# Kernel tuning notes

Measured on AMD Instinct MI355X. Metric: run time of the kernel, lower is better.

## Reference

```python
import jax, jax.numpy as jnp
import numpy as np

EPS = 1e-7  # K.epsilon()
ROUTINGS = 3

def squash(v, axis=-1):
    s2 = jnp.sum(jnp.square(v), axis=axis, keepdims=True)
    scale = s2 / (1.0 + s2) / jnp.sqrt(s2 + EPS)
    return scale * v

def setup_inputs() -> dict:
    key = jax.random.key(0)
    k1, k2 = jax.random.split(key)
    B, N, I = 128, 512, 256   # batch, input_num_capsule, input_dim_capsule
    M, D = 32, 16             # num_capsule, dim_capsule
    x = jax.random.normal(k1, (B, N, I), dtype=jnp.float32)
    W = jax.random.normal(k2, (M, N, D, I), dtype=jnp.float32) * 0.05
    return {"x": x, "W": W}

def reference(x, W):
    # x: [B,N,I], W: [M,N,D,I]
    # inputs_hat[b,m,n,d] = sum_i x[b,n,i] * W[m,n,d,i]
    inputs_hat = jnp.einsum('bni,mndi->bmnd', x, W)
    B, M, N, _ = inputs_hat.shape
    b = jnp.zeros((B, M, N), dtype=inputs_hat.dtype)
    outputs = None
    for i in range(ROUTINGS):
        c = jax.nn.softmax(b, axis=1)  # softmax over num_capsule dim (dim=1)
        s = jnp.einsum('bmn,bmnd->bmd', c, inputs_hat)
        outputs = squash(s)
        if i < ROUTINGS - 1:
            b = b + jnp.einsum('bmd,bmnd->bmn', outputs, inputs_hat)
    return outputs
```

## Files before the change

kernel.cpp:

```cpp
#include <hip/hip_runtime.h>
#include <stdint.h>

#define B_ 128
#define N_ 512
#define I_ 256
#define M_ 32
#define D_ 16

typedef __attribute__((ext_vector_type(4))) float f32x4;
typedef __attribute__((ext_vector_type(4))) float float4v;
typedef __attribute__((ext_vector_type(8))) short short8;
typedef __attribute__((ext_vector_type(2))) unsigned int u32x2;
typedef __attribute__((ext_vector_type(4))) unsigned int u32x4;
typedef unsigned short ushort;

__device__ __forceinline__ float bf2f(ushort u) {
    union { unsigned int i; float f; } v; v.i = ((unsigned int)u) << 16; return v.f;
}
__device__ __forceinline__ ushort f2bf(float f) {
    union { float f; unsigned int i; } v; v.f = f;
    unsigned int r = v.i + 0x7FFFu + ((v.i >> 16) & 1u);
    return (ushort)(r >> 16);
}

__device__ __forceinline__ short8 cvt8(float4v lo, float4v hi) {
    unsigned int u0, u1, u2, u3;
    asm("v_cvt_pk_bf16_f32 %0, %1, %2" : "=v"(u0) : "v"(lo[0]), "v"(lo[1]));
    asm("v_cvt_pk_bf16_f32 %0, %1, %2" : "=v"(u1) : "v"(lo[2]), "v"(lo[3]));
    asm("v_cvt_pk_bf16_f32 %0, %1, %2" : "=v"(u2) : "v"(hi[0]), "v"(hi[1]));
    asm("v_cvt_pk_bf16_f32 %0, %1, %2" : "=v"(u3) : "v"(hi[2]), "v"(hi[3]));
    u32x4 uv = {u0, u1, u2, u3};
    return __builtin_bit_cast(short8, uv);
}
__device__ __forceinline__ u32x2 cvt4(float4v v) {
    unsigned int u0, u1;
    asm("v_cvt_pk_bf16_f32 %0, %1, %2" : "=v"(u0) : "v"(v[0]), "v"(v[1]));
    asm("v_cvt_pk_bf16_f32 %0, %1, %2" : "=v"(u1) : "v"(v[2]), "v"(v[3]));
    u32x2 r = {u0, u1};
    return r;
}

#define GL16(dst, base, imm) \
    asm volatile("global_load_dwordx4 %0, %1, off offset:%2" \
                 : "=&v"(dst) : "v"(base), "n"(imm))

#define VMW0() do { \
    asm volatile("s_waitcnt vmcnt(0)" ::: "memory"); \
    __builtin_amdgcn_sched_barrier(0); \
} while (0)

__global__ __launch_bounds__(512, 2) void hat_gemm(const float* __restrict__ x,
                                                   const float* __restrict__ W,
                                                   ushort* __restrict__ hat) {
    __shared__ ushort LDS[32768];

    const int bid = blockIdx.x;
    const int n   = (bid & 7) * 64 + (bid >> 3);

    const int tid  = threadIdx.x;
    const int lane = tid & 63;
    const int w    = tid >> 6;
    const int l15  = lane & 15;
    const int kq   = lane >> 4;

    {
        const int row = tid >> 2;
        const int seg = tid & 3;
        const float* xp = x + ((size_t)row * N_ + n) * I_ + seg * 64;
        float4v sx[16];
        #pragma unroll
        for (int j = 0; j < 16; ++j) GL16(sx[j], xp, j * 16);
        VMW0();
        #pragma unroll
        for (int i = 0; i < 8; ++i) {
            short8 h = cvt8(sx[2 * i], sx[2 * i + 1]);
            const int gsw = (seg * 8 + i) ^ (row & 15);
            *(short8*)&LDS[row * 256 + gsw * 8] = h;
        }
    }
    __syncthreads();

    short8 afr[8];
    #pragma unroll
    for (int ks = 0; ks < 8; ++ks)
        afr[ks] = *(const short8*)&LDS[(w * 16 + l15) * 256 + (((ks * 4 + kq) ^ l15) * 8)];

    float4v sv[8];

    #define ISSUEW(c) do { \
        _Pragma("unroll") \
        for (int u = 0; u < 8; ++u) { \
            const int rr = w * 8 + u;           \
            const int ml = rr >> 4, dd = rr & 15; \
            const float* wp = W + ((((size_t)((c) * 4 + ml)) * N_ + n) * D_ + dd) * I_ + lane * 4; \
            GL16(sv[u], wp, 0); \
        } \
    } while (0)

    #define WRITEW(c) do { \
        ushort* buf = &LDS[((c) & 1) * 16384]; \
        _Pragma("unroll") \
        for (int u = 0; u < 8; ++u) { \
            const int rr = w * 8 + u; \
            const int dd = rr & 15; \
            u32x2 h = cvt4(sv[u]); \
            *(u32x2*)&buf[rr * 256 + (((lane >> 1) ^ dd) * 8) + (lane & 1) * 4] = h; \
        } \
    } while (0)

    ISSUEW(0);
    __syncthreads();
    VMW0();
    WRITEW(0);
    __syncthreads();

    for (int c = 0; c < 8; ++c) {
        if (c < 7) ISSUEW(c + 1);
        const ushort* buf = &LDS[(c & 1) * 16384];
        #pragma unroll
        for (int mq = 0; mq < 4; ++mq) {
            const int m = c * 4 + mq;
            f32x4 acc = {0.f, 0.f, 0.f, 0.f};
            #pragma unroll
            for (int ks = 0; ks < 8; ++ks) {
                short8 bf = *(const short8*)&buf[(mq * 16 + l15) * 256 + (((ks * 4 + kq) ^ l15) * 8)];
                acc = __builtin_amdgcn_mfma_f32_16x16x32_bf16(afr[ks], bf, acc, 0, 0, 0);
            }
            #pragma unroll
            for (int r = 0; r < 4; ++r) {
                const int b = w * 16 + kq * 4 + r;
                hat[(((size_t)b * M_ + m) * N_ + n) * D_ + l15] = f2bf(acc[r]);
            }
        }
        if (c < 7) {
            VMW0();
            WRITEW(c + 1);
            __syncthreads();
        }
    }
    #undef ISSUEW
    #undef WRITEW
}

__global__ __launch_bounds__(512) void routing(const ushort* __restrict__ hat,
                                               float* __restrict__ out) {
    __shared__ float blog[M_][N_];
    __shared__ float cmax[N_];
    __shared__ float rcsum[N_];

    const int b    = blockIdx.x;
    const int tid  = threadIdx.x;
    const int lane = tid & 63;
    const int w    = tid >> 6;

    #pragma unroll
    for (int m = 0; m < M_; ++m) blog[m][tid] = 0.f;
    __syncthreads();

    float ov[4][16];
    typedef __attribute__((ext_vector_type(4))) float fl4;

    for (int it = 0; it < 3; ++it) {
        {
            float mx = -3.4e38f;
            #pragma unroll
            for (int m = 0; m < M_; ++m) mx = fmaxf(mx, blog[m][tid]);
            float s = 0.f;
            #pragma unroll
            for (int m = 0; m < M_; ++m) s += __expf(blog[m][tid] - mx);
            cmax[tid]  = mx;
            rcsum[tid] = 1.f / s;
        }
        __syncthreads();

        float sacc[4][16];
        #pragma unroll
        for (int q = 0; q < 4; ++q)
            #pragma unroll
            for (int dd = 0; dd < 16; ++dd) sacc[q][dd] = 0.f;

        for (int r = 0; r < 8; ++r) {
            const int nn = r * 64 + lane;
            #pragma unroll
            for (int q = 0; q < 4; ++q) {
                const int m = w * 4 + q;
                const float cm = __expf(blog[m][nn] - cmax[nn]) * rcsum[nn];
                const size_t base = (((size_t)b * M_ + m) * N_ + nn) * D_;
                short8 h0 = *(const short8*)(hat + base);
                short8 h1 = *(const short8*)(hat + base + 8);
                #pragma unroll
                for (int dd = 0; dd < 8; ++dd) {
                    sacc[q][dd]     += cm * bf2f((ushort)h0[dd]);
                    sacc[q][8 + dd] += cm * bf2f((ushort)h1[dd]);
                }
            }
        }
        #pragma unroll
        for (int off = 32; off >= 1; off >>= 1) {
            #pragma unroll
            for (int q = 0; q < 4; ++q)
                #pragma unroll
                for (int dd = 0; dd < 16; ++dd)
                    sacc[q][dd] += __shfl_xor(sacc[q][dd], off, 64);
        }
        #pragma unroll
        for (int q = 0; q < 4; ++q) {
            float s2 = 0.f;
            #pragma unroll
            for (int dd = 0; dd < 16; ++dd) s2 += sacc[q][dd] * sacc[q][dd];
            const float scale = s2 / (1.f + s2) / sqrtf(s2 + 1e-7f);
            #pragma unroll
            for (int dd = 0; dd < 16; ++dd) ov[q][dd] = scale * sacc[q][dd];
        }

        if (it < 2) {
            for (int r = 0; r < 8; ++r) {
                const int nn = r * 64 + lane;
                #pragma unroll
                for (int q = 0; q < 4; ++q) {
                    const int m = w * 4 + q;
                    const size_t base = (((size_t)b * M_ + m) * N_ + nn) * D_;
                    short8 h0 = *(const short8*)(hat + base);
                    short8 h1 = *(const short8*)(hat + base + 8);
                    float dot = 0.f;
                    #pragma unroll
                    for (int dd = 0; dd < 8; ++dd) {
                        dot += ov[q][dd]     * bf2f((ushort)h0[dd]);
                        dot += ov[q][8 + dd] * bf2f((ushort)h1[dd]);
                    }
                    blog[m][nn] += dot;
                }
            }
        }
        __syncthreads();
    }

    if (lane == 0) {
        #pragma unroll
        for (int q = 0; q < 4; ++q) {
            const int m = w * 4 + q;
            #pragma unroll
            for (int c4 = 0; c4 < 4; ++c4) {
                fl4 v;
                v[0] = ov[q][c4 * 4 + 0];
                v[1] = ov[q][c4 * 4 + 1];
                v[2] = ov[q][c4 * 4 + 2];
                v[3] = ov[q][c4 * 4 + 3];
                *(fl4*)&out[((size_t)b * M_ + m) * D_ + c4 * 4] = v;
            }
        }
    }
}

extern "C" void kernel_launch(void* const* d_in, const int* in_sizes, int n_in,
                              void* d_out, int out_size, void* d_ws, size_t ws_size,
                              hipStream_t stream) {
    const float* x = (const float*)d_in[0];
    const float* W = (const float*)d_in[1];
    ushort* hat = (ushort*)d_ws;
    float* out = (float*)d_out;

    hat_gemm<<<dim3(N_), dim3(512), 0, stream>>>(x, W, hat);
    routing<<<dim3(B_), dim3(512), 0, stream>>>(hat, out);
}
```

Baseline: 161.3 us.

## Pre-convert x to bf16 transposed and loop n per block in hat GEMM

Adds a separate conv_x kernel that casts x to bf16 and lays it out as [N][B][I]. hat_gemm now launches 256 blocks, each handling one m-quarter across 16 consecutive n, and prefetches the next n's x and W tiles while computing the current one. This halves the x bytes the GEMM reads and removes the per-block fp32 load and convert of x. In exchange it adds an extra kernel launch, an extra global write and read of xT, and four times the total x reads across m-quarters, with one block per CU instead of two.

```diff
diff --git a/kernel.cpp b/kernel.cpp
--- a/kernel.cpp
+++ b/kernel.cpp
@@ -12,6 +12,7 @@
 typedef __attribute__((ext_vector_type(8))) short short8;
 typedef __attribute__((ext_vector_type(2))) unsigned int u32x2;
 typedef __attribute__((ext_vector_type(4))) unsigned int u32x4;
+typedef __attribute__((ext_vector_type(4))) unsigned short ushort4v;
 typedef unsigned short ushort;
 
 __device__ __forceinline__ float bf2f(ushort u) {
@@ -23,15 +24,6 @@
     return (ushort)(r >> 16);
 }
 
-__device__ __forceinline__ short8 cvt8(float4v lo, float4v hi) {
-    unsigned int u0, u1, u2, u3;
-    asm("v_cvt_pk_bf16_f32 %0, %1, %2" : "=v"(u0) : "v"(lo[0]), "v"(lo[1]));
-    asm("v_cvt_pk_bf16_f32 %0, %1, %2" : "=v"(u1) : "v"(lo[2]), "v"(lo[3]));
-    asm("v_cvt_pk_bf16_f32 %0, %1, %2" : "=v"(u2) : "v"(hi[0]), "v"(hi[1]));
-    asm("v_cvt_pk_bf16_f32 %0, %1, %2" : "=v"(u3) : "v"(hi[2]), "v"(hi[3]));
-    u32x4 uv = {u0, u1, u2, u3};
-    return __builtin_bit_cast(short8, uv);
-}
 __device__ __forceinline__ u32x2 cvt4(float4v v) {
     unsigned int u0, u1;
     asm("v_cvt_pk_bf16_f32 %0, %1, %2" : "=v"(u0) : "v"(v[0]), "v"(v[1]));
@@ -40,22 +32,37 @@
     return r;
 }
 
-#define GL16(dst, base, imm) \
-    asm volatile("global_load_dwordx4 %0, %1, off offset:%2" \
-                 : "=&v"(dst) : "v"(base), "n"(imm))
+#define GL16(dst, ptr) \
+    asm volatile("global_load_dwordx4 %0, %1, off" : "=&v"(dst) : "v"(ptr))
 
 #define VMW0() do { \
     asm volatile("s_waitcnt vmcnt(0)" ::: "memory"); \
     __builtin_amdgcn_sched_barrier(0); \
 } while (0)
 
-__global__ __launch_bounds__(512, 2) void hat_gemm(const float* __restrict__ x,
-                                                   const float* __restrict__ W,
+__global__ __launch_bounds__(256) void conv_x(const float* __restrict__ x,
+                                              ushort* __restrict__ xT) {
+    const int rid = blockIdx.x * 4 + (threadIdx.x >> 6);
+    const int i0  = (threadIdx.x & 63) * 4;
+    const int b   = rid >> 9;
+    const int n   = rid & 511;
+    float4v v = *(const float4v*)(x + (size_t)rid * I_ + i0);
+    ushort4v h;
+    h[0] = f2bf(v[0]); h[1] = f2bf(v[1]); h[2] = f2bf(v[2]); h[3] = f2bf(v[3]);
+    *(ushort4v*)(xT + ((size_t)(n * B_ + b)) * I_ + i0) = h;
+}
+
+__global__ __launch_bounds__(512, 1) void hat_gemm(const float* __restrict__ W,
+                                                   const ushort* __restrict__ xT,
                                                    ushort* __restrict__ hat) {
-    __shared__ ushort LDS[32768];
-
-    const int bid = blockIdx.x;
-    const int n   = (bid & 7) * 64 + (bid >> 3);
+    __shared__ ushort LDSa[32768];
+    __shared__ ushort LDSw[16384];
+
+    const int bid  = blockIdx.x;
+    const int xcd  = bid & 7;
+    const int idx  = bid >> 3;
+    const int nc   = xcd * 4 + (idx & 3);
+    const int mq   = idx >> 2;
 
     const int tid  = threadIdx.x;
     const int lane = tid & 63;
@@ -63,83 +70,77 @@
     const int l15  = lane & 15;
     const int kq   = lane >> 4;
 
-    {
-        const int row = tid >> 2;
-        const int seg = tid & 3;
-        const float* xp = x + ((size_t)row * N_ + n) * I_ + seg * 64;
-        float4v sx[16];
-        #pragma unroll
-        for (int j = 0; j < 16; ++j) GL16(sx[j], xp, j * 16);
-        VMW0();
-        #pragma unroll
-        for (int i = 0; i < 8; ++i) {
-            short8 h = cvt8(sx[2 * i], sx[2 * i + 1]);
-            const int gsw = (seg * 8 + i) ^ (row & 15);
-            *(short8*)&LDS[row * 256 + gsw * 8] = h;
-        }
-    }
-    __syncthreads();
-
-    short8 afr[8];
-    #pragma unroll
-    for (int ks = 0; ks < 8; ++ks)
-        afr[ks] = *(const short8*)&LDS[(w * 16 + l15) * 256 + (((ks * 4 + kq) ^ l15) * 8)];
-
-    float4v sv[8];
-
-    #define ISSUEW(c) do { \
+    short8  sva[8];
+    float4v svw[8];
+
+    const int rowAl = (lane >> 5);
+    const int gA    = lane & 31;
+
+    #define ISSUE_A(n) do { \
+        const ushort* xTn = xT + (size_t)(n) * (B_ * I_) + (size_t)(w * 16) * I_ + lane * 8; \
+        _Pragma("unroll") \
+        for (int j = 0; j < 8; ++j) GL16(sva[j], xTn + (size_t)j * 2 * I_); \
+    } while (0)
+
+    #define ISSUE_W(n) do { \
         _Pragma("unroll") \
         for (int u = 0; u < 8; ++u) { \
-            const int rr = w * 8 + u;           \
-            const int ml = rr >> 4, dd = rr & 15; \
-            const float* wp = W + ((((size_t)((c) * 4 + ml)) * N_ + n) * D_ + dd) * I_ + lane * 4; \
-            GL16(sv[u], wp, 0); \
+            const int rr = w * 8 + u; \
+            const float* wp = W + ((((size_t)(mq * 4 + (rr >> 4))) * N_ + (n)) * D_ + (rr & 15)) * I_ + lane * 4; \
+            GL16(svw[u], wp); \
         } \
     } while (0)
 
-    #define WRITEW(c) do { \
-        ushort* buf = &LDS[((c) & 1) * 16384]; \
+    #define WRITE_AW() do { \
+        _Pragma("unroll") \
+        for (int j = 0; j < 8; ++j) { \
+            const int rowA = w * 16 + j * 2 + rowAl; \
+            *(short8*)&LDSa[rowA * 256 + ((gA ^ (rowA & 15)) * 8)] = sva[j]; \
+        } \
         _Pragma("unroll") \
         for (int u = 0; u < 8; ++u) { \
             const int rr = w * 8 + u; \
-            const int dd = rr & 15; \
-            u32x2 h = cvt4(sv[u]); \
-            *(u32x2*)&buf[rr * 256 + (((lane >> 1) ^ dd) * 8) + (lane & 1) * 4] = h; \
+            u32x2 h = cvt4(svw[u]); \
+            *(u32x2*)&LDSw[rr * 256 + (((lane >> 1) ^ (rr & 15)) * 8) + (lane & 1) * 4] = h; \
         } \
     } while (0)
 
-    ISSUEW(0);
-    __syncthreads();
-    VMW0();
-    WRITEW(0);
-    __syncthreads();
-
-    for (int c = 0; c < 8; ++c) {
-        if (c < 7) ISSUEW(c + 1);
-        const ushort* buf = &LDS[(c & 1) * 16384];
-        #pragma unroll
-        for (int mq = 0; mq < 4; ++mq) {
-            const int m = c * 4 + mq;
+    ISSUE_A(nc * 16); ISSUE_W(nc * 16);
+
+    for (int ni = 0; ni < 16; ++ni) {
+        const int n = nc * 16 + ni;
+
+        VMW0();
+        WRITE_AW();
+        __syncthreads();
+
+        if (ni < 15) { ISSUE_A(n + 1); ISSUE_W(n + 1); }
+
+        short8 afr[8];
+        #pragma unroll
+        for (int ks = 0; ks < 8; ++ks)
+            afr[ks] = *(const short8*)&LDSa[(w * 16 + l15) * 256 + (((ks * 4 + kq) ^ l15) * 8)];
+
+        #pragma unroll
+        for (int ml = 0; ml < 4; ++ml) {
             f32x4 acc = {0.f, 0.f, 0.f, 0.f};
             #pragma unroll
             for (int ks = 0; ks < 8; ++ks) {
-                short8 bf = *(const short8*)&buf[(mq * 16 + l15) * 256 + (((ks * 4 + kq) ^ l15) * 8)];
+                short8 bf = *(const short8*)&LDSw[(ml * 16 + l15) * 256 + (((ks * 4 + kq) ^ l15) * 8)];
                 acc = __builtin_amdgcn_mfma_f32_16x16x32_bf16(afr[ks], bf, acc, 0, 0, 0);
             }
+            const int m = mq * 4 + ml;
             #pragma unroll
             for (int r = 0; r < 4; ++r) {
                 const int b = w * 16 + kq * 4 + r;
                 hat[(((size_t)b * M_ + m) * N_ + n) * D_ + l15] = f2bf(acc[r]);
             }
         }
-        if (c < 7) {
-            VMW0();
-            WRITEW(c + 1);
-            __syncthreads();
-        }
+        __syncthreads();
     }
-    #undef ISSUEW
-    #undef WRITEW
+    #undef ISSUE_A
+    #undef ISSUE_W
+    #undef WRITE_AW
 }
 
 __global__ __launch_bounds__(512) void routing(const ushort* __restrict__ hat,
@@ -258,8 +259,10 @@
     const float* x = (const float*)d_in[0];
     const float* W = (const float*)d_in[1];
     ushort* hat = (ushort*)d_ws;
+    ushort* xT  = (ushort*)((char*)d_ws + (size_t)64 * 1024 * 1024);
     float* out = (float*)d_out;
 
-    hat_gemm<<<dim3(N_), dim3(512), 0, stream>>>(x, W, hat);
+    conv_x<<<dim3((B_ * N_) / 4), dim3(256), 0, stream>>>(x, xT);
+    hat_gemm<<<dim3(256), dim3(512), 0, stream>>>(W, xT, hat);
     routing<<<dim3(B_), dim3(512), 0, stream>>>(hat, out);
 }
```

Measured after the change: 188.3 us. 16.8% more time.

## Fuse routing logit update with softmax and weighted sum to reuse hat loads

Applied to the files above, without the earlier changes.

Restructures the routing kernel so each routing iteration reads inputs_hat once. The agreement dot-product update, the per-column softmax over capsules and the next weighted sum are done in the same pass over each 64-column chunk, keeping the loaded hat values in registers. The first iteration uses the constant uniform coefficient 1/32 instead of a softmax over zeros. This cuts global reads of hat from five passes to three. In exchange it adds a __syncthreads per chunk, recomputes the max and sum over all 32 capsules redundantly in every wave, and raises register pressure, which launch_bounds(512,1) is meant to accommodate.

```diff
diff --git a/kernel.cpp b/kernel.cpp
--- a/kernel.cpp
+++ b/kernel.cpp
@@ -90,7 +90,7 @@
     #define ISSUEW(c) do { \
         _Pragma("unroll") \
         for (int u = 0; u < 8; ++u) { \
-            const int rr = w * 8 + u;           \
+            const int rr = w * 8 + u; \
             const int ml = rr >> 4, dd = rr & 15; \
             const float* wp = W + ((((size_t)((c) * 4 + ml)) * N_ + n) * D_ + dd) * I_ + lane * 4; \
             GL16(sv[u], wp, 0); \
@@ -142,11 +142,9 @@
     #undef WRITEW
 }
 
-__global__ __launch_bounds__(512) void routing(const ushort* __restrict__ hat,
-                                               float* __restrict__ out) {
+__global__ __launch_bounds__(512, 1) void routing(const ushort* __restrict__ hat,
+                                                  float* __restrict__ out) {
     __shared__ float blog[M_][N_];
-    __shared__ float cmax[N_];
-    __shared__ float rcsum[N_];
 
     const int b    = blockIdx.x;
     const int tid  = threadIdx.x;
@@ -157,23 +155,53 @@
     for (int m = 0; m < M_; ++m) blog[m][tid] = 0.f;
     __syncthreads();
 
-    float ov[4][16];
+    float ov[4][16], sacc[4][16];
     typedef __attribute__((ext_vector_type(4))) float fl4;
 
-    for (int it = 0; it < 3; ++it) {
-        {
-            float mx = -3.4e38f;
-            #pragma unroll
-            for (int m = 0; m < M_; ++m) mx = fmaxf(mx, blog[m][tid]);
-            float s = 0.f;
-            #pragma unroll
-            for (int m = 0; m < M_; ++m) s += __expf(blog[m][tid] - mx);
-            cmax[tid]  = mx;
-            rcsum[tid] = 1.f / s;
-        }
-        __syncthreads();
-
-        float sacc[4][16];
+    #define REDUCE_SQUASH() do { \
+        _Pragma("unroll") \
+        for (int off = 32; off >= 1; off >>= 1) { \
+            _Pragma("unroll") \
+            for (int q = 0; q < 4; ++q) \
+                _Pragma("unroll") \
+                for (int dd = 0; dd < 16; ++dd) \
+                    sacc[q][dd] += __shfl_xor(sacc[q][dd], off, 64); \
+        } \
+        _Pragma("unroll") \
+        for (int q = 0; q < 4; ++q) { \
+            float s2 = 0.f; \
+            _Pragma("unroll") \
+            for (int dd = 0; dd < 16; ++dd) s2 += sacc[q][dd] * sacc[q][dd]; \
+            const float scale = s2 / (1.f + s2) / sqrtf(s2 + 1e-7f); \
+            _Pragma("unroll") \
+            for (int dd = 0; dd < 16; ++dd) ov[q][dd] = scale * sacc[q][dd]; \
+        } \
+    } while (0)
+
+    #pragma unroll
+    for (int q = 0; q < 4; ++q)
+        #pragma unroll
+        for (int dd = 0; dd < 16; ++dd) sacc[q][dd] = 0.f;
+
+    for (int r = 0; r < 8; ++r) {
+        const int nn = r * 64 + lane;
+        #pragma unroll
+        for (int q = 0; q < 4; ++q) {
+            const int m = w * 4 + q;
+            const size_t base = (((size_t)b * M_ + m) * N_ + nn) * D_;
+            short8 h0 = *(const short8*)(hat + base);
+            short8 h1 = *(const short8*)(hat + base + 8);
+            const float cm = 0.03125f;
+            #pragma unroll
+            for (int dd = 0; dd < 8; ++dd) {
+                sacc[q][dd]     += cm * bf2f((ushort)h0[dd]);
+                sacc[q][8 + dd] += cm * bf2f((ushort)h1[dd]);
+            }
+        }
+    }
+    REDUCE_SQUASH();
+
+    for (int t = 0; t < 2; ++t) {
         #pragma unroll
         for (int q = 0; q < 4; ++q)
             #pragma unroll
@@ -181,59 +209,42 @@
 
         for (int r = 0; r < 8; ++r) {
             const int nn = r * 64 + lane;
+            short8 hh0[4], hh1[4];
             #pragma unroll
             for (int q = 0; q < 4; ++q) {
                 const int m = w * 4 + q;
-                const float cm = __expf(blog[m][nn] - cmax[nn]) * rcsum[nn];
                 const size_t base = (((size_t)b * M_ + m) * N_ + nn) * D_;
-                short8 h0 = *(const short8*)(hat + base);
-                short8 h1 = *(const short8*)(hat + base + 8);
+                hh0[q] = *(const short8*)(hat + base);
+                hh1[q] = *(const short8*)(hat + base + 8);
+                float dot = 0.f;
                 #pragma unroll
                 for (int dd = 0; dd < 8; ++dd) {
-                    sacc[q][dd]     += cm * bf2f((ushort)h0[dd]);
-                    sacc[q][8 + dd] += cm * bf2f((ushort)h1[dd]);
+                    dot += ov[q][dd]     * bf2f((ushort)hh0[q][dd]);
+                    dot += ov[q][8 + dd] * bf2f((ushort)hh1[q][dd]);
                 }
-            }
-        }
-        #pragma unroll
-        for (int off = 32; off >= 1; off >>= 1) {
-            #pragma unroll
-            for (int q = 0; q < 4; ++q)
+                blog[m][nn] += dot;
+            }
+            __syncthreads();
+            float mx = -3.4e38f;
+            #pragma unroll
+            for (int mm = 0; mm < M_; ++mm) mx = fmaxf(mx, blog[mm][nn]);
+            float ss = 0.f;
+            #pragma unroll
+            for (int mm = 0; mm < M_; ++mm) ss += __expf(blog[mm][nn] - mx);
+            const float rs = 1.f / ss;
+            #pragma unroll
+            for (int q = 0; q < 4; ++q) {
+                const float cm = __expf(blog[w * 4 + q][nn] - mx) * rs;
                 #pragma unroll
-                for (int dd = 0; dd < 16; ++dd)
-                    sacc[q][dd] += __shfl_xor(sacc[q][dd], off, 64);
-        }
-        #pragma unroll
-        for (int q = 0; q < 4; ++q) {
-            float s2 = 0.f;
-            #pragma unroll
-            for (int dd = 0; dd < 16; ++dd) s2 += sacc[q][dd] * sacc[q][dd];
-            const float scale = s2 / (1.f + s2) / sqrtf(s2 + 1e-7f);
-            #pragma unroll
-            for (int dd = 0; dd < 16; ++dd) ov[q][dd] = scale * sacc[q][dd];
-        }
-
-        if (it < 2) {
-            for (int r = 0; r < 8; ++r) {
-                const int nn = r * 64 + lane;
-                #pragma unroll
-                for (int q = 0; q < 4; ++q) {
-                    const int m = w * 4 + q;
-                    const size_t base = (((size_t)b * M_ + m) * N_ + nn) * D_;
-                    short8 h0 = *(const short8*)(hat + base);
-                    short8 h1 = *(const short8*)(hat + base + 8);
-                    float dot = 0.f;
-                    #pragma unroll
-                    for (int dd = 0; dd < 8; ++dd) {
-                        dot += ov[q][dd]     * bf2f((ushort)h0[dd]);
-                        dot += ov[q][8 + dd] * bf2f((ushort)h1[dd]);
-                    }
-                    blog[m][nn] += dot;
+                for (int dd = 0; dd < 8; ++dd) {
+                    sacc[q][dd]     += cm * bf2f((ushort)hh0[q][dd]);
+                    sacc[q][8 + dd] += cm * bf2f((ushort)hh1[q][dd]);
                 }
             }
         }
-        __syncthreads();
-    }
+        REDUCE_SQUASH();
+    }
+    #undef REDUCE_SQUASH
 
     if (lane == 0) {
         #pragma unroll
```

Measured after the change: 165.7 us. 2.8% more time.
